# Performance work log

Hardware: AMD Instinct MI355X
Metric: run time of the kernel (lower is better)

The kernel has to match this reference:

```python
import jax, jax.numpy as jnp
import numpy as np
from jax import lax

B, BERT_DIM, Z_DIM, ODE_UNITS, T_MAX = 4096, 768, 64, 128, 512
LN_EPS = 1e-5

def _glorot(key, shape):
    fan_in, fan_out = shape[0], shape[1]
    lim = float(np.sqrt(6.0 / (fan_in + fan_out)))
    return jax.random.uniform(key, shape, jnp.float32, -lim, lim)

def setup_inputs() -> dict:
    key = jax.random.key(0)
    ks = jax.random.split(key, 16)
    inp = {
        'bert_emb': jax.random.normal(ks[0], (B, BERT_DIM), jnp.float32),
        'times': jax.random.uniform(ks[1], (B, T_MAX), jnp.float32),
        'seq_lens': jax.random.randint(ks[2], (B,), 0, T_MAX).astype(jnp.int64),
        'eps': jax.random.normal(ks[3], (B, Z_DIM), jnp.float32),
        # bert_proj: Linear(768->64) + LayerNorm(64)
        'proj_W': _glorot(ks[4], (BERT_DIM, Z_DIM)),
        'proj_b': jnp.zeros((Z_DIM,), jnp.float32),
        'ln_g': jnp.ones((Z_DIM,), jnp.float32),
        'ln_b': jnp.zeros((Z_DIM,), jnp.float32),
        # DiffusionAug
        'log_noise_std': jnp.float32(-2.0),
        'den_W1': _glorot(ks[5], (Z_DIM, 2 * Z_DIM)),
        'den_b1': jnp.zeros((2 * Z_DIM,), jnp.float32),
        'den_W2': _glorot(ks[6], (2 * Z_DIM, Z_DIM)),
        'den_b2': jnp.zeros((Z_DIM,), jnp.float32),
        # ODEFunc: Linear->Tanh->Linear->Tanh->Linear (xavier_uniform, zero bias)
        'ode_W1': _glorot(ks[7], (Z_DIM, ODE_UNITS)),
        'ode_b1': jnp.zeros((ODE_UNITS,), jnp.float32),
        'ode_W2': _glorot(ks[8], (ODE_UNITS, ODE_UNITS)),
        'ode_b2': jnp.zeros((ODE_UNITS,), jnp.float32),
        'ode_W3': _glorot(ks[9], (ODE_UNITS, Z_DIM)),
        'ode_b3': jnp.zeros((Z_DIM,), jnp.float32),
        # dec_head: Linear(64->2)
        'dec_W': _glorot(ks[10], (Z_DIM, 2)),
        'dec_b': jnp.zeros((2,), jnp.float32),
    }
    return inp

def reference(bert_emb, times, seq_lens, eps, proj_W, proj_b, ln_g, ln_b,
              log_noise_std, den_W1, den_b1, den_W2, den_b2,
              ode_W1, ode_b1, ode_W2, ode_b2, ode_W3, ode_b3, dec_W, dec_b):
    T = times.shape[1]
    # bert_proj: Linear + LayerNorm (dropout = identity in eval)
    h = bert_emb @ proj_W + proj_b
    mu = jnp.mean(h, axis=-1, keepdims=True)
    var = jnp.var(h, axis=-1, keepdims=True)
    z_clean = (h - mu) * lax.rsqrt(var + LN_EPS) * ln_g + ln_b
    # DiffusionAug: noise + denoise MLP, MSE to detached clean latent
    sigma = jax.nn.softplus(log_noise_std)
    z_noisy = z_clean + sigma * eps
    z_aug = jax.nn.silu(z_noisy @ den_W1 + den_b1) @ den_W2 + den_b2
    diff_loss = jnp.mean((z_aug - lax.stop_gradient(z_clean)) ** 2)
    # Euler ODE integration: z <- z + dt * f(z), T sequential steps
    dt = jnp.float32(1.0 / max(T, 1))
    def step(z, _):
        f = jnp.tanh(jnp.tanh(z @ ode_W1 + ode_b1) @ ode_W2 + ode_b2) @ ode_W3 + ode_b3
        z_new = z + dt * f
        return z_new, z_new
    _, zs = lax.scan(step, z_aug, None, length=T)  # zs: (T, B, z)
    traj = jnp.concatenate([z_aug[:, None, :], jnp.swapaxes(zs, 0, 1)], axis=1)  # (B, T+1, z)
    out = traj @ dec_W + dec_b  # (B, T+1, 2)
    pred_delta = out[:, :, 0]
    stop_logits = out[:, :, 1]
    return (pred_delta, stop_logits, diff_loss)
```

## Files before the change

kernel.cpp:

```cpp
#include <hip/hip_runtime.h>
#include <stdint.h>

#define NB 4096
#define NT 512
#define OT 513
#define TOTE (NB*OT)
#define LOSSOFF (2*TOTE)

typedef float  f32x4 __attribute__((ext_vector_type(4)));
typedef __fp16 f16x8 __attribute__((ext_vector_type(8)));
typedef __fp16 f16x2 __attribute__((ext_vector_type(2)));

#define MFMA(A,B,C) __builtin_amdgcn_mfma_f32_16x16x32_f16((A),(B),(C),0,0,0)

__device__ __forceinline__ void wg_barrier() {
  asm volatile("s_waitcnt lgkmcnt(0)\n\ts_barrier" ::: "memory");
}

__device__ __forceinline__ float fast_tanh(float x) {
  float e = __builtin_amdgcn_exp2f(x * 2.8853900817779268f);
  return __builtin_fmaf(-2.0f, __builtin_amdgcn_rcpf(1.0f + e), 1.0f);
}
__device__ __forceinline__ float fast_silu(float x) {
  float e = __builtin_amdgcn_exp2f(x * -1.4426950408889634f);
  return x * __builtin_amdgcn_rcpf(1.0f + e);
}
__device__ __forceinline__ uint32_t pk2(float a, float b) {
  union { f16x2 h; uint32_t u; } c;
  c.h = __builtin_amdgcn_cvt_pkrtz(a, b);
  return c.u;
}
__device__ __forceinline__ f16x8 pack8(f32x4 a, f32x4 b) {
  union { f16x8 v; f16x2 h[4]; } u;
  u.h[0] = __builtin_amdgcn_cvt_pkrtz(a.x, a.y);
  u.h[1] = __builtin_amdgcn_cvt_pkrtz(a.z, a.w);
  u.h[2] = __builtin_amdgcn_cvt_pkrtz(b.x, b.y);
  u.h[3] = __builtin_amdgcn_cvt_pkrtz(b.z, b.w);
  return u.v;
}

#define WS_WPAK (1u<<20)
#define WS_UBUF ((1u<<20) + (256u<<10))
#define WS_CBUF ((1u<<20) + (384u<<10))

__global__ void compose_kernel(const float* __restrict__ oW1, const float* __restrict__ oW3,
                               const float* __restrict__ ob3, const float* __restrict__ dW,
                               float* __restrict__ Ubuf, float* __restrict__ cbuf,
                               float* __restrict__ dout) {
  int g = blockIdx.x, tid = threadIdx.x;
  if (g < 72) {
    int e = g * 256 + tid;
    int i = e / 144, j = e - i * 144;
    float s = 0.f;
    if (j < 128) {
      #pragma unroll 4
      for (int k = 0; k < 64; k++) s = __builtin_fmaf(oW3[i * 64 + k], oW1[k * 128 + j], s);
    } else if (j < 130) {
      int cc = j - 128;
      for (int k = 0; k < 64; k++) s = __builtin_fmaf(oW3[i * 64 + k], dW[k * 2 + cc], s);
    }
    Ubuf[i * 144 + j] = s;
  } else {
    if (tid < 144) {
      float s = 0.f;
      if (tid < 128) {
        for (int k = 0; k < 64; k++) s = __builtin_fmaf(ob3[k], oW1[k * 128 + tid], s);
      } else if (tid < 130) {
        int cc = tid - 128;
        for (int k = 0; k < 64; k++) s = __builtin_fmaf(ob3[k], dW[k * 2 + cc], s);
      }
      cbuf[tid] = s;
    }
    if (tid == 255) dout[LOSSOFF] = 0.0f;
  }
}

__global__ void pack_kernel(const float* __restrict__ oW1, const float* __restrict__ oW2,
                            const float* __restrict__ dW,  const float* __restrict__ dW1,
                            const float* __restrict__ dW2, const float* __restrict__ pW,
                            const float* __restrict__ Ubuf, char* __restrict__ wdst) {
  int g = blockIdx.x * 256 + threadIdx.x;
  int fid = g >> 6, lane = g & 63;
  if (fid >= 228 || (fid >= 50 && fid < 64)) return;
  int m4 = lane & 15;
  if (fid >= 48 && fid < 50) {
    int kt = fid - 48;
    int k0 = kt * 32 + (lane >> 4) * 8;
    f16x8 out;
    #pragma unroll
    for (int j = 0; j < 8; j++) out[j] = (m4 < 2) ? (__fp16)dW[(k0 + j) * 2 + m4] : (__fp16)0.f;
    *(f16x8*)(wdst + (size_t)(fid * 64 + lane) * 16) = out;
    return;
  }
  const float* src; int Kt, M, base;
  if      (fid < 16)  { src = oW1;  Kt = 2;  M = 128; base = 0;   }
  else if (fid < 48)  { src = oW2;  Kt = 4;  M = 128; base = 16;  }
  else if (fid < 80)  { src = dW1;  Kt = 2;  M = 128; base = 64;  }
  else if (fid < 96)  { src = dW2;  Kt = 4;  M = 64;  base = 80;  }
  else if (fid < 192) { src = pW;   Kt = 24; M = 64;  base = 96;  }
  else                { src = Ubuf; Kt = 4;  M = 144; base = 192; }
  int local = fid - base;
  int mt = local / Kt, kt = local % Kt;
  int m  = mt * 16 + m4;
  int k0 = kt * 32 + (lane >> 4) * 8;
  f16x8 out;
  #pragma unroll
  for (int j = 0; j < 8; j++) out[j] = (__fp16)src[(size_t)(k0 + j) * M + m];
  *(f16x8*)(wdst + (size_t)(fid * 64 + lane) * 16) = out;
}

__global__ __launch_bounds__(512, 2) void prologue_kernel(
    const float* __restrict__ bert, const float* __restrict__ eps,
    const float* __restrict__ projb, const float* __restrict__ lng,
    const float* __restrict__ lnb,  const float* __restrict__ lns,
    const float* __restrict__ db1,  const float* __restrict__ db2,
    const char* __restrict__ wpack, float* __restrict__ wsz,
    float* __restrict__ dout) {
  __shared__ __attribute__((aligned(16))) char sZ[16 * 128];
  __shared__ __attribute__((aligned(16))) char sH[16 * 256];
  __shared__ f32x4  sScr[4 * 64];
  __shared__ float2 sMV[64];
  __shared__ float  sLsum[4];

  const int tid  = threadIdx.x;
  const int wave = tid >> 6, lane = tid & 63;
  const int q = lane >> 4, b = lane & 15;
  const int bg = blockIdx.x * 16 + b;
  const int b7 = b & 7;
  const f16x8* wp = (const f16x8*)wpack;
  const int u0 = wave * 16 + q * 4;

  const int zr0 = b * 128 + ((q    ) ^ b7) * 16;
  const int zr1 = b * 128 + ((q + 4) ^ b7) * 16;
  int hr[4];
  #pragma unroll
  for (int s = 0; s < 4; s++) hr[s] = b * 256 + ((4 * s + q) ^ b7) * 16;
  const int hw = b * 256 + (((2 * wave + (q >> 1)) ^ b7) * 16) + (q & 1) * 8;
  const int zw = b * 128 + (((2 * (wave & 3) + (q >> 1)) ^ b7) * 16) + (q & 1) * 8;

  const int mt = wave & 3, kh = wave >> 2;
  f32x4 hA = {0,0,0,0}, hB = {0,0,0,0};
  #pragma unroll 4
  for (int i = 0; i < 12; i++) {
    int kt = kh * 12 + i;
    f16x8 af = wp[(size_t)(96 + mt * 24 + kt) * 64 + lane];
    const float* bp = bert + (size_t)bg * 768 + kt * 32 + q * 8;
    f32x4 f0 = *(const f32x4*)bp;
    f32x4 f1 = *(const f32x4*)(bp + 4);
    f16x8 bf = pack8(f0, f1);
    if (i & 1) hB = MFMA(af, bf, hB); else hA = MFMA(af, bf, hA);
  }
  f32x4 hacc = hA + hB;
  if (wave >= 4) sScr[(wave - 4) * 64 + lane] = hacc;
  __syncthreads();

  f32x4 h = {0,0,0,0}, zc = {0,0,0,0};
  if (wave < 4) {
    h = hacc + sScr[wave * 64 + lane];
    h.x += projb[u0 + 0]; h.y += projb[u0 + 1];
    h.z += projb[u0 + 2]; h.w += projb[u0 + 3];
    float s1 = h.x + h.y + h.z + h.w;
    float s2 = h.x*h.x + h.y*h.y + h.z*h.z + h.w*h.w;
    s1 += __shfl_xor(s1, 16); s1 += __shfl_xor(s1, 32);
    s2 += __shfl_xor(s2, 16); s2 += __shfl_xor(s2, 32);
    if (q == 0) sMV[wave * 16 + b] = make_float2(s1, s2);
  }
  __syncthreads();
  if (wave < 4) {
    float t1 = 0.f, t2 = 0.f;
    #pragma unroll
    for (int w2 = 0; w2 < 4; w2++) { float2 m = sMV[w2 * 16 + b]; t1 += m.x; t2 += m.y; }
    float mu  = t1 * (1.0f / 64.0f);
    float var = t2 * (1.0f / 64.0f) - mu * mu;
    float rs  = rsqrtf(var + 1e-5f);
    float sigma = logf(1.0f + expf(lns[0]));
    f32x4 e = *(const f32x4*)(eps + (size_t)bg * 64 + u0);
    zc.x = __builtin_fmaf((h.x - mu) * rs, lng[u0+0], lnb[u0+0]);
    zc.y = __builtin_fmaf((h.y - mu) * rs, lng[u0+1], lnb[u0+1]);
    zc.z = __builtin_fmaf((h.z - mu) * rs, lng[u0+2], lnb[u0+2]);
    zc.w = __builtin_fmaf((h.w - mu) * rs, lng[u0+3], lnb[u0+3]);
    f32x4 zn = zc + sigma * e;
    *(uint2*)(sZ + zw) = make_uint2(pk2(zn.x, zn.y), pk2(zn.z, zn.w));
  }
  __syncthreads();
  {
    f16x8 w0 = wp[(size_t)(64 + wave * 2 + 0) * 64 + lane];
    f16x8 w1 = wp[(size_t)(64 + wave * 2 + 1) * 64 + lane];
    f16x8 bz0 = *(const f16x8*)(sZ + zr0);
    f16x8 bz1 = *(const f16x8*)(sZ + zr1);
    f32x4 bias = { db1[u0+0], db1[u0+1], db1[u0+2], db1[u0+3] };
    f32x4 acc = MFMA(w0, bz0, bias);
    acc = MFMA(w1, bz1, acc);
    *(uint2*)(sH + hw) = make_uint2(pk2(fast_silu(acc.x), fast_silu(acc.y)),
                                    pk2(fast_silu(acc.z), fast_silu(acc.w)));
  }
  __syncthreads();
  if (wave < 4) {
    f16x8 w0 = wp[(size_t)(80 + wave * 4 + 0) * 64 + lane];
    f16x8 w1 = wp[(size_t)(80 + wave * 4 + 1) * 64 + lane];
    f16x8 w2 = wp[(size_t)(80 + wave * 4 + 2) * 64 + lane];
    f16x8 w3 = wp[(size_t)(80 + wave * 4 + 3) * 64 + lane];
    f16x8 g0 = *(const f16x8*)(sH + hr[0]);
    f16x8 g1 = *(const f16x8*)(sH + hr[1]);
    f16x8 g2 = *(const f16x8*)(sH + hr[2]);
    f16x8 g3 = *(const f16x8*)(sH + hr[3]);
    f32x4 bias = { db2[u0+0], db2[u0+1], db2[u0+2], db2[u0+3] };
    const f32x4 z4 = {0,0,0,0};
    f32x4 aA = MFMA(w0, g0, bias); aA = MFMA(w1, g1, aA);
    f32x4 aB = MFMA(w2, g2, z4);   aB = MFMA(w3, g3, aB);
    f32x4 za = aA + aB;
    *(f32x4*)(wsz + (size_t)bg * 64 + u0) = za;
    f32x4 d = za - zc;
    float sl = d.x*d.x + d.y*d.y + d.z*d.z + d.w*d.w;
    const int offs[6] = {1, 2, 4, 8, 16, 32};
    #pragma unroll
    for (int i = 0; i < 6; i++) sl += __shfl_xor(sl, offs[i]);
    if (lane == 0) sLsum[wave] = sl;
  }
  __syncthreads();
  if (tid == 0)
    atomicAdd(dout + LOSSOFF,
              (sLsum[0] + sLsum[1] + sLsum[2] + sLsum[3]) * (1.0f / 262144.0f));
}

__global__ __launch_bounds__(512, 1) void ode_kernel(
    const float* __restrict__ wsz, const char* __restrict__ wpack,
    const float* __restrict__ ob1, const float* __restrict__ cbuf,
    const float* __restrict__ ob2, const float* __restrict__ decb,
    float* __restrict__ dout) {
  __shared__ __attribute__((aligned(16))) char sH1[4096];
  __shared__ __attribute__((aligned(16))) char sH2[4096];

  const int tid  = threadIdx.x;
  const int wave = tid >> 6, lane = tid & 63;
  const int q = lane >> 4, b = lane & 15;
  const f16x8* wp = (const f16x8*)wpack;
  const float dtc = 1.0f / 512.0f;
  const f32x4 zero4 = {0,0,0,0};

  int rd[4];
  #pragma unroll
  for (int kt = 0; kt < 4; kt++) rd[kt] = b * 256 + (((kt * 4 + q) ^ b) * 16);
  const int wr = b * 256 + (((wave * 2 + (q >> 1)) ^ b) * 16) + (q & 1) * 8;

  f16x8 w2f[4], uf[4], uf8[4];
  #pragma unroll
  for (int kt = 0; kt < 4; kt++) {
    w2f[kt] = wp[(size_t)(16  + wave * 4 + kt) * 64 + lane];
    uf [kt] = wp[(size_t)(192 + wave * 4 + kt) * 64 + lane];
  }
  if (wave == 7) {
    #pragma unroll
    for (int kt = 0; kt < 4; kt++)
      uf8[kt] = wp[(size_t)(192 + 32 + kt) * 64 + lane];
  }
  const f32x4 b2f = *(const f32x4*)(ob2  + wave * 16 + q * 4);
  const f32x4 cw  = *(const f32x4*)(cbuf + wave * 16 + q * 4);
  const f32x4 c8  = *(const f32x4*)(cbuf + 128 + q * 4);

  const int bg = blockIdx.x * 16 + b;
  const float* zrow = wsz + (size_t)bg * 64;
  f32x4 z0a = *(const f32x4*)(zrow + q * 8);
  f32x4 z0b = *(const f32x4*)(zrow + q * 8 + 4);
  f32x4 z1a = *(const f32x4*)(zrow + 32 + q * 8);
  f32x4 z1b = *(const f32x4*)(zrow + 32 + q * 8 + 4);
  f16x8 zf0 = pack8(z0a, z0b);
  f16x8 zf1 = pack8(z1a, z1b);

  f32x4 b1v = *(const f32x4*)(ob1 + wave * 16 + q * 4);
  f32x4 G = MFMA(wp[(size_t)(wave * 2 + 0) * 64 + lane], zf0, b1v);
  G = MFMA(wp[(size_t)(wave * 2 + 1) * 64 + lane], zf1, G);
  *(uint2*)(sH1 + wr) = make_uint2(pk2(fast_tanh(G.x), fast_tanh(G.y)),
                                   pk2(fast_tanh(G.z), fast_tanh(G.w)));

  f32x4 Gd = zero4;
  float* const outp_p = dout + (size_t)bg * OT;
  float* const outp_s = dout + (size_t)TOTE + (size_t)bg * OT;
  if (wave == 7) {
    f32x4 b1d = zero4;
    if (q == 0) { b1d.x = decb[0]; b1d.y = decb[1]; }
    Gd = MFMA(wp[(size_t)48 * 64 + lane], zf0, b1d);
    Gd = MFMA(wp[(size_t)49 * 64 + lane], zf1, Gd);
    if (q == 0) { outp_p[0] = Gd.x; outp_s[0] = Gd.y; }
  }
  wg_barrier();

  #pragma unroll 1
  for (int t = 0; t < NT; ++t) {
    f16x8 p0 = *(const f16x8*)(sH1 + rd[0]);
    f16x8 p1 = *(const f16x8*)(sH1 + rd[1]);
    f16x8 p2 = *(const f16x8*)(sH1 + rd[2]);
    f16x8 p3 = *(const f16x8*)(sH1 + rd[3]);
    f32x4 a  = MFMA(w2f[0], p0, b2f);
    a  = MFMA(w2f[1], p1, a);
    f32x4 a2 = MFMA(w2f[2], p2, zero4);
    a2 = MFMA(w2f[3], p3, a2);
    f32x4 hv = a + a2;
    *(uint2*)(sH2 + wr) = make_uint2(pk2(fast_tanh(hv.x), fast_tanh(hv.y)),
                                     pk2(fast_tanh(hv.z), fast_tanh(hv.w)));
    wg_barrier();

    f16x8 g0 = *(const f16x8*)(sH2 + rd[0]);
    f16x8 g1 = *(const f16x8*)(sH2 + rd[1]);
    f16x8 g2 = *(const f16x8*)(sH2 + rd[2]);
    f16x8 g3 = *(const f16x8*)(sH2 + rd[3]);
    f32x4 d  = MFMA(uf[0], g0, cw);
    d  = MFMA(uf[1], g1, d);
    f32x4 d2 = MFMA(uf[2], g2, zero4);
    d2 = MFMA(uf[3], g3, d2);
    G.x = __builtin_fmaf(dtc, d.x + d2.x, G.x);
    G.y = __builtin_fmaf(dtc, d.y + d2.y, G.y);
    G.z = __builtin_fmaf(dtc, d.z + d2.z, G.z);
    G.w = __builtin_fmaf(dtc, d.w + d2.w, G.w);
    *(uint2*)(sH1 + wr) = make_uint2(pk2(fast_tanh(G.x), fast_tanh(G.y)),
                                     pk2(fast_tanh(G.z), fast_tanh(G.w)));
    if (wave == 7) {
      f32x4 e  = MFMA(uf8[0], g0, c8);
      e  = MFMA(uf8[1], g1, e);
      f32x4 e2 = MFMA(uf8[2], g2, zero4);
      e2 = MFMA(uf8[3], g3, e2);
      Gd.x = __builtin_fmaf(dtc, e.x + e2.x, Gd.x);
      Gd.y = __builtin_fmaf(dtc, e.y + e2.y, Gd.y);
      if (q == 0) { outp_p[t + 1] = Gd.x; outp_s[t + 1] = Gd.y; }
    }
    wg_barrier();
  }
}

extern "C" void kernel_launch(void* const* d_in, const int* in_sizes, int n_in,
                              void* d_out, int out_size, void* d_ws, size_t ws_size,
                              hipStream_t stream) {
  const float* bert  = (const float*)d_in[0];
  const float* eps   = (const float*)d_in[3];
  const float* projW = (const float*)d_in[4];
  const float* projb = (const float*)d_in[5];
  const float* lng   = (const float*)d_in[6];
  const float* lnb   = (const float*)d_in[7];
  const float* lns   = (const float*)d_in[8];
  const float* denW1 = (const float*)d_in[9];
  const float* denb1 = (const float*)d_in[10];
  const float* denW2 = (const float*)d_in[11];
  const float* denb2 = (const float*)d_in[12];
  const float* odeW1 = (const float*)d_in[13];
  const float* odeb1 = (const float*)d_in[14];
  const float* odeW2 = (const float*)d_in[15];
  const float* odeb2 = (const float*)d_in[16];
  const float* odeW3 = (const float*)d_in[17];
  const float* odeb3 = (const float*)d_in[18];
  const float* decW  = (const float*)d_in[19];
  const float* decb  = (const float*)d_in[20];
  float* dout = (float*)d_out;

  float* wsz  = (float*)d_ws;
  char*  wpak = (char*)d_ws + WS_WPAK;
  float* Ubuf = (float*)((char*)d_ws + WS_UBUF);
  float* cbuf = (float*)((char*)d_ws + WS_CBUF);

  compose_kernel<<<73, 256, 0, stream>>>(odeW1, odeW3, odeb3, decW, Ubuf, cbuf, dout);
  pack_kernel<<<57, 256, 0, stream>>>(odeW1, odeW2, decW, denW1, denW2, projW, Ubuf, wpak);
  prologue_kernel<<<256, 512, 0, stream>>>(bert, eps, projb, lng, lnb, lns,
                                           denb1, denb2, wpak, wsz, dout);
  ode_kernel<<<256, 512, 0, stream>>>(wsz, wpak, odeb1, cbuf, odeb2, decb, dout);
}
```

Baseline: 428.5 us.

## Halve ODE block waves with two tiles per wave and fold dt into weights

The ODE kernel now runs 4 waves per block instead of 8, and each wave handles two 16-row output tiles. This cuts barrier participants and gives each wave independent MFMA chains it can interleave. The Euler step size dt is pre-multiplied into the composed U matrix and the c bias in compose_kernel. That lets the MFMA accumulate straight into the carried state G, which removes the per-step FMA scaling. The cost is more registers per wave, and the scaled fp16 weights lose some precision because small values may drop toward the subnormal range.

```diff
diff --git a/kernel.cpp b/kernel.cpp
--- a/kernel.cpp
+++ b/kernel.cpp
@@ -47,6 +47,7 @@
                                const float* __restrict__ ob3, const float* __restrict__ dW,
                                float* __restrict__ Ubuf, float* __restrict__ cbuf,
                                float* __restrict__ dout) {
+  const float dtc = 1.0f / 512.0f;
   int g = blockIdx.x, tid = threadIdx.x;
   if (g < 72) {
     int e = g * 256 + tid;
@@ -59,7 +60,7 @@
       int cc = j - 128;
       for (int k = 0; k < 64; k++) s = __builtin_fmaf(oW3[i * 64 + k], dW[k * 2 + cc], s);
     }
-    Ubuf[i * 144 + j] = s;
+    Ubuf[i * 144 + j] = s * dtc;
   } else {
     if (tid < 144) {
       float s = 0.f;
@@ -69,7 +70,7 @@
         int cc = tid - 128;
         for (int k = 0; k < 64; k++) s = __builtin_fmaf(ob3[k], dW[k * 2 + cc], s);
       }
-      cbuf[tid] = s;
+      cbuf[tid] = s * dtc;
     }
     if (tid == 255) dout[LOSSOFF] = 0.0f;
   }
@@ -223,7 +224,7 @@
               (sLsum[0] + sLsum[1] + sLsum[2] + sLsum[3]) * (1.0f / 262144.0f));
 }
 
-__global__ __launch_bounds__(512, 1) void ode_kernel(
+__global__ __launch_bounds__(256, 1) void ode_kernel(
     const float* __restrict__ wsz, const char* __restrict__ wpack,
     const float* __restrict__ ob1, const float* __restrict__ cbuf,
     const float* __restrict__ ob2, const float* __restrict__ decb,
@@ -235,28 +236,37 @@
   const int wave = tid >> 6, lane = tid & 63;
   const int q = lane >> 4, b = lane & 15;
   const f16x8* wp = (const f16x8*)wpack;
-  const float dtc = 1.0f / 512.0f;
   const f32x4 zero4 = {0,0,0,0};
 
   int rd[4];
   #pragma unroll
   for (int kt = 0; kt < 4; kt++) rd[kt] = b * 256 + (((kt * 4 + q) ^ b) * 16);
-  const int wr = b * 256 + (((wave * 2 + (q >> 1)) ^ b) * 16) + (q & 1) * 8;
-
-  f16x8 w2f[4], uf[4], uf8[4];
-  #pragma unroll
-  for (int kt = 0; kt < 4; kt++) {
-    w2f[kt] = wp[(size_t)(16  + wave * 4 + kt) * 64 + lane];
-    uf [kt] = wp[(size_t)(192 + wave * 4 + kt) * 64 + lane];
-  }
-  if (wave == 7) {
+  int wr[2];
+  #pragma unroll
+  for (int t2 = 0; t2 < 2; t2++)
+    wr[t2] = b * 256 + (((4 * wave + 2 * t2 + (q >> 1)) ^ b) * 16) + (q & 1) * 8;
+
+  f16x8 w2f[8], uf[8], uf8[4];
+  #pragma unroll
+  for (int t2 = 0; t2 < 2; t2++)
+    #pragma unroll
+    for (int kt = 0; kt < 4; kt++) {
+      w2f[t2 * 4 + kt] = wp[(size_t)(16  + (2 * wave + t2) * 4 + kt) * 64 + lane];
+      uf [t2 * 4 + kt] = wp[(size_t)(192 + (2 * wave + t2) * 4 + kt) * 64 + lane];
+    }
+  if (wave == 3) {
     #pragma unroll
     for (int kt = 0; kt < 4; kt++)
       uf8[kt] = wp[(size_t)(192 + 32 + kt) * 64 + lane];
   }
-  const f32x4 b2f = *(const f32x4*)(ob2  + wave * 16 + q * 4);
-  const f32x4 cw  = *(const f32x4*)(cbuf + wave * 16 + q * 4);
-  const f32x4 c8  = *(const f32x4*)(cbuf + 128 + q * 4);
+  f32x4 b2f[2], cw[2];
+  #pragma unroll
+  for (int t2 = 0; t2 < 2; t2++) {
+    int u0t = (2 * wave + t2) * 16 + q * 4;
+    b2f[t2] = *(const f32x4*)(ob2  + u0t);
+    cw [t2] = *(const f32x4*)(cbuf + u0t);
+  }
+  const f32x4 c8 = *(const f32x4*)(cbuf + 128 + q * 4);
 
   const int bg = blockIdx.x * 16 + b;
   const float* zrow = wsz + (size_t)bg * 64;
@@ -267,16 +277,21 @@
   f16x8 zf0 = pack8(z0a, z0b);
   f16x8 zf1 = pack8(z1a, z1b);
 
-  f32x4 b1v = *(const f32x4*)(ob1 + wave * 16 + q * 4);
-  f32x4 G = MFMA(wp[(size_t)(wave * 2 + 0) * 64 + lane], zf0, b1v);
-  G = MFMA(wp[(size_t)(wave * 2 + 1) * 64 + lane], zf1, G);
-  *(uint2*)(sH1 + wr) = make_uint2(pk2(fast_tanh(G.x), fast_tanh(G.y)),
-                                   pk2(fast_tanh(G.z), fast_tanh(G.w)));
-
+  f32x4 G[2];
+  #pragma unroll
+  for (int t2 = 0; t2 < 2; t2++) {
+    int mt = 2 * wave + t2;
+    f32x4 b1v = *(const f32x4*)(ob1 + mt * 16 + q * 4);
+    f32x4 d = MFMA(wp[(size_t)(mt * 2 + 0) * 64 + lane], zf0, b1v);
+    d = MFMA(wp[(size_t)(mt * 2 + 1) * 64 + lane], zf1, d);
+    G[t2] = d;
+    *(uint2*)(sH1 + wr[t2]) = make_uint2(pk2(fast_tanh(d.x), fast_tanh(d.y)),
+                                         pk2(fast_tanh(d.z), fast_tanh(d.w)));
+  }
   f32x4 Gd = zero4;
   float* const outp_p = dout + (size_t)bg * OT;
   float* const outp_s = dout + (size_t)TOTE + (size_t)bg * OT;
-  if (wave == 7) {
+  if (wave == 3) {
     f32x4 b1d = zero4;
     if (q == 0) { b1d.x = decb[0]; b1d.y = decb[1]; }
     Gd = MFMA(wp[(size_t)48 * 64 + lane], zf0, b1d);
@@ -291,36 +306,39 @@
     f16x8 p1 = *(const f16x8*)(sH1 + rd[1]);
     f16x8 p2 = *(const f16x8*)(sH1 + rd[2]);
     f16x8 p3 = *(const f16x8*)(sH1 + rd[3]);
-    f32x4 a  = MFMA(w2f[0], p0, b2f);
-    a  = MFMA(w2f[1], p1, a);
-    f32x4 a2 = MFMA(w2f[2], p2, zero4);
-    a2 = MFMA(w2f[3], p3, a2);
-    f32x4 hv = a + a2;
-    *(uint2*)(sH2 + wr) = make_uint2(pk2(fast_tanh(hv.x), fast_tanh(hv.y)),
-                                     pk2(fast_tanh(hv.z), fast_tanh(hv.w)));
+    #pragma unroll
+    for (int t2 = 0; t2 < 2; t2++) {
+      f32x4 a  = MFMA(w2f[t2*4+0], p0, b2f[t2]);
+      a  = MFMA(w2f[t2*4+1], p1, a);
+      f32x4 a2 = MFMA(w2f[t2*4+2], p2, zero4);
+      a2 = MFMA(w2f[t2*4+3], p3, a2);
+      f32x4 hv = a + a2;
+      *(uint2*)(sH2 + wr[t2]) = make_uint2(pk2(fast_tanh(hv.x), fast_tanh(hv.y)),
+                                           pk2(fast_tanh(hv.z), fast_tanh(hv.w)));
+    }
     wg_barrier();
 
     f16x8 g0 = *(const f16x8*)(sH2 + rd[0]);
     f16x8 g1 = *(const f16x8*)(sH2 + rd[1]);
     f16x8 g2 = *(const f16x8*)(sH2 + rd[2]);
     f16x8 g3 = *(const f16x8*)(sH2 + rd[3]);
-    f32x4 d  = MFMA(uf[0], g0, cw);
-    d  = MFMA(uf[1], g1, d);
-    f32x4 d2 = MFMA(uf[2], g2, zero4);
-    d2 = MFMA(uf[3], g3, d2);
-    G.x = __builtin_fmaf(dtc, d.x + d2.x, G.x);
-    G.y = __builtin_fmaf(dtc, d.y + d2.y, G.y);
-    G.z = __builtin_fmaf(dtc, d.z + d2.z, G.z);
-    G.w = __builtin_fmaf(dtc, d.w + d2.w, G.w);
-    *(uint2*)(sH1 + wr) = make_uint2(pk2(fast_tanh(G.x), fast_tanh(G.y)),
-                                     pk2(fast_tanh(G.z), fast_tanh(G.w)));
-    if (wave == 7) {
-      f32x4 e  = MFMA(uf8[0], g0, c8);
+    #pragma unroll
+    for (int t2 = 0; t2 < 2; t2++) {
+      f32x4 d  = MFMA(uf[t2*4+0], g0, G[t2]);
+      d  = MFMA(uf[t2*4+1], g1, d);
+      f32x4 d2 = MFMA(uf[t2*4+2], g2, zero4);
+      d2 = MFMA(uf[t2*4+3], g3, d2);
+      f32x4 Gn = d + d2 + cw[t2];
+      G[t2] = Gn;
+      *(uint2*)(sH1 + wr[t2]) = make_uint2(pk2(fast_tanh(Gn.x), fast_tanh(Gn.y)),
+                                           pk2(fast_tanh(Gn.z), fast_tanh(Gn.w)));
+    }
+    if (wave == 3) {
+      f32x4 e  = MFMA(uf8[0], g0, Gd);
       e  = MFMA(uf8[1], g1, e);
       f32x4 e2 = MFMA(uf8[2], g2, zero4);
       e2 = MFMA(uf8[3], g3, e2);
-      Gd.x = __builtin_fmaf(dtc, e.x + e2.x, Gd.x);
-      Gd.y = __builtin_fmaf(dtc, e.y + e2.y, Gd.y);
+      Gd = e + e2 + c8;
       if (q == 0) { outp_p[t + 1] = Gd.x; outp_s[t + 1] = Gd.y; }
     }
     wg_barrier();
@@ -360,5 +378,5 @@
   pack_kernel<<<57, 256, 0, stream>>>(odeW1, odeW2, decW, denW1, denW2, projW, Ubuf, wpak);
   prologue_kernel<<<256, 512, 0, stream>>>(bert, eps, projb, lng, lnb, lns,
                                            denb1, denb2, wpak, wsz, dout);
-  ode_kernel<<<256, 512, 0, stream>>>(wsz, wpak, odeb1, cbuf, odeb2, decb, dout);
-}
+  ode_kernel<<<256, 256, 0, stream>>>(wsz, wpak, odeb1, cbuf, odeb2, decb, dout);
+}
```

New measurement: 499.0 us. 16.4% more time.

## Fuse prep and main kernels, fold dt into composed weights, keep z in LDS

Applied to the files above, without the earlier changes.

Merges the compose and pack kernels into one prep kernel that computes the dt-scaled composed W3·W1 weights directly into packed fp16 form. The prologue and ODE kernels are fused, so the augmented latent is passed through shared memory instead of a global round-trip. The Euler update is folded into the MFMA accumulator by pre-scaling the weights and bias with dt, which removes per-step FMAs. The goal is fewer launches and less memory traffic. The cost is more fp16 rounding on the small scaled weights and on the stored latent.

```diff
diff --git a/kernel.cpp b/kernel.cpp
--- a/kernel.cpp
+++ b/kernel.cpp
@@ -39,28 +39,17 @@
   return u.v;
 }
 
-#define WS_WPAK (1u<<20)
-#define WS_UBUF ((1u<<20) + (256u<<10))
-#define WS_CBUF ((1u<<20) + (384u<<10))
-
-__global__ void compose_kernel(const float* __restrict__ oW1, const float* __restrict__ oW3,
-                               const float* __restrict__ ob3, const float* __restrict__ dW,
-                               float* __restrict__ Ubuf, float* __restrict__ cbuf,
-                               float* __restrict__ dout) {
-  int g = blockIdx.x, tid = threadIdx.x;
-  if (g < 72) {
-    int e = g * 256 + tid;
-    int i = e / 144, j = e - i * 144;
-    float s = 0.f;
-    if (j < 128) {
-      #pragma unroll 4
-      for (int k = 0; k < 64; k++) s = __builtin_fmaf(oW3[i * 64 + k], oW1[k * 128 + j], s);
-    } else if (j < 130) {
-      int cc = j - 128;
-      for (int k = 0; k < 64; k++) s = __builtin_fmaf(oW3[i * 64 + k], dW[k * 2 + cc], s);
-    }
-    Ubuf[i * 144 + j] = s;
-  } else {
+#define WS_CBUF (256u<<10)
+
+__global__ void prep_kernel(const float* __restrict__ oW1, const float* __restrict__ oW2,
+                            const float* __restrict__ dW,  const float* __restrict__ dW1,
+                            const float* __restrict__ dW2, const float* __restrict__ pW,
+                            const float* __restrict__ oW3, const float* __restrict__ ob3,
+                            char* __restrict__ wdst, float* __restrict__ cbuf,
+                            float* __restrict__ dout) {
+  const float dtc = 1.0f / 512.0f;
+  if (blockIdx.x == 57) {
+    int tid = threadIdx.x;
     if (tid < 144) {
       float s = 0.f;
       if (tid < 128) {
@@ -69,58 +58,77 @@
         int cc = tid - 128;
         for (int k = 0; k < 64; k++) s = __builtin_fmaf(ob3[k], dW[k * 2 + cc], s);
       }
-      cbuf[tid] = s;
+      cbuf[tid] = s * dtc;
     }
     if (tid == 255) dout[LOSSOFF] = 0.0f;
-  }
-}
-
-__global__ void pack_kernel(const float* __restrict__ oW1, const float* __restrict__ oW2,
-                            const float* __restrict__ dW,  const float* __restrict__ dW1,
-                            const float* __restrict__ dW2, const float* __restrict__ pW,
-                            const float* __restrict__ Ubuf, char* __restrict__ wdst) {
+    return;
+  }
   int g = blockIdx.x * 256 + threadIdx.x;
   int fid = g >> 6, lane = g & 63;
-  if (fid >= 228 || (fid >= 50 && fid < 64)) return;
+  if (fid >= 50 && fid < 64) return;
   int m4 = lane & 15;
+  int k0 = (lane >> 4) * 8;
   if (fid >= 48 && fid < 50) {
     int kt = fid - 48;
-    int k0 = kt * 32 + (lane >> 4) * 8;
+    int kb = kt * 32 + k0;
     f16x8 out;
     #pragma unroll
-    for (int j = 0; j < 8; j++) out[j] = (m4 < 2) ? (__fp16)dW[(k0 + j) * 2 + m4] : (__fp16)0.f;
+    for (int j = 0; j < 8; j++) out[j] = (m4 < 2) ? (__fp16)dW[(kb + j) * 2 + m4] : (__fp16)0.f;
     *(f16x8*)(wdst + (size_t)(fid * 64 + lane) * 16) = out;
     return;
   }
+  if (fid >= 192) {
+    int local = fid - 192;
+    int mt = local >> 2, kt = local & 3;
+    int m  = mt * 16 + m4;
+    int kb = kt * 32 + k0;
+    f16x8 out;
+    #pragma unroll
+    for (int j = 0; j < 8; j++) {
+      int k = kb + j;
+      float s = 0.f;
+      if (m < 128) {
+        #pragma unroll 4
+        for (int i = 0; i < 64; i++) s = __builtin_fmaf(oW3[k * 64 + i], oW1[i * 128 + m], s);
+      } else if (m < 130) {
+        for (int i = 0; i < 64; i++) s = __builtin_fmaf(oW3[k * 64 + i], dW[i * 2 + (m - 128)], s);
+      }
+      out[j] = (__fp16)(s * dtc);
+    }
+    *(f16x8*)(wdst + (size_t)(fid * 64 + lane) * 16) = out;
+    return;
+  }
   const float* src; int Kt, M, base;
-  if      (fid < 16)  { src = oW1;  Kt = 2;  M = 128; base = 0;   }
-  else if (fid < 48)  { src = oW2;  Kt = 4;  M = 128; base = 16;  }
-  else if (fid < 80)  { src = dW1;  Kt = 2;  M = 128; base = 64;  }
-  else if (fid < 96)  { src = dW2;  Kt = 4;  M = 64;  base = 80;  }
-  else if (fid < 192) { src = pW;   Kt = 24; M = 64;  base = 96;  }
-  else                { src = Ubuf; Kt = 4;  M = 144; base = 192; }
+  if      (fid < 16)  { src = oW1;  Kt = 2;  M = 128; base = 0;  }
+  else if (fid < 48)  { src = oW2;  Kt = 4;  M = 128; base = 16; }
+  else if (fid < 80)  { src = dW1;  Kt = 2;  M = 128; base = 64; }
+  else if (fid < 96)  { src = dW2;  Kt = 4;  M = 64;  base = 80; }
+  else                { src = pW;   Kt = 24; M = 64;  base = 96; }
   int local = fid - base;
   int mt = local / Kt, kt = local % Kt;
   int m  = mt * 16 + m4;
-  int k0 = kt * 32 + (lane >> 4) * 8;
+  int kb = kt * 32 + k0;
   f16x8 out;
   #pragma unroll
-  for (int j = 0; j < 8; j++) out[j] = (__fp16)src[(size_t)(k0 + j) * M + m];
+  for (int j = 0; j < 8; j++) out[j] = (__fp16)src[(size_t)(kb + j) * M + m];
   *(f16x8*)(wdst + (size_t)(fid * 64 + lane) * 16) = out;
 }
 
-__global__ __launch_bounds__(512, 2) void prologue_kernel(
+__global__ __launch_bounds__(512, 1) void main_kernel(
     const float* __restrict__ bert, const float* __restrict__ eps,
     const float* __restrict__ projb, const float* __restrict__ lng,
     const float* __restrict__ lnb,  const float* __restrict__ lns,
     const float* __restrict__ db1,  const float* __restrict__ db2,
-    const char* __restrict__ wpack, float* __restrict__ wsz,
-    float* __restrict__ dout) {
+    const float* __restrict__ ob1,  const float* __restrict__ ob2,
+    const float* __restrict__ decb, const char* __restrict__ wpack,
+    const float* __restrict__ cbuf, float* __restrict__ dout) {
   __shared__ __attribute__((aligned(16))) char sZ[16 * 128];
   __shared__ __attribute__((aligned(16))) char sH[16 * 256];
   __shared__ f32x4  sScr[4 * 64];
   __shared__ float2 sMV[64];
   __shared__ float  sLsum[4];
+  __shared__ __attribute__((aligned(16))) char sH1[4096];
+  __shared__ __attribute__((aligned(16))) char sH2[4096];
 
   const int tid  = threadIdx.x;
   const int wave = tid >> 6, lane = tid & 63;
@@ -129,6 +137,7 @@
   const int b7 = b & 7;
   const f16x8* wp = (const f16x8*)wpack;
   const int u0 = wave * 16 + q * 4;
+  const f32x4 zero4 = {0,0,0,0};
 
   const int zr0 = b * 128 + ((q    ) ^ b7) * 16;
   const int zr1 = b * 128 + ((q + 4) ^ b7) * 16;
@@ -138,105 +147,90 @@
   const int hw = b * 256 + (((2 * wave + (q >> 1)) ^ b7) * 16) + (q & 1) * 8;
   const int zw = b * 128 + (((2 * (wave & 3) + (q >> 1)) ^ b7) * 16) + (q & 1) * 8;
 
-  const int mt = wave & 3, kh = wave >> 2;
-  f32x4 hA = {0,0,0,0}, hB = {0,0,0,0};
-  #pragma unroll 4
-  for (int i = 0; i < 12; i++) {
-    int kt = kh * 12 + i;
-    f16x8 af = wp[(size_t)(96 + mt * 24 + kt) * 64 + lane];
-    const float* bp = bert + (size_t)bg * 768 + kt * 32 + q * 8;
-    f32x4 f0 = *(const f32x4*)bp;
-    f32x4 f1 = *(const f32x4*)(bp + 4);
-    f16x8 bf = pack8(f0, f1);
-    if (i & 1) hB = MFMA(af, bf, hB); else hA = MFMA(af, bf, hA);
-  }
-  f32x4 hacc = hA + hB;
-  if (wave >= 4) sScr[(wave - 4) * 64 + lane] = hacc;
-  __syncthreads();
-
-  f32x4 h = {0,0,0,0}, zc = {0,0,0,0};
-  if (wave < 4) {
-    h = hacc + sScr[wave * 64 + lane];
-    h.x += projb[u0 + 0]; h.y += projb[u0 + 1];
-    h.z += projb[u0 + 2]; h.w += projb[u0 + 3];
-    float s1 = h.x + h.y + h.z + h.w;
-    float s2 = h.x*h.x + h.y*h.y + h.z*h.z + h.w*h.w;
-    s1 += __shfl_xor(s1, 16); s1 += __shfl_xor(s1, 32);
-    s2 += __shfl_xor(s2, 16); s2 += __shfl_xor(s2, 32);
-    if (q == 0) sMV[wave * 16 + b] = make_float2(s1, s2);
-  }
-  __syncthreads();
-  if (wave < 4) {
-    float t1 = 0.f, t2 = 0.f;
-    #pragma unroll
-    for (int w2 = 0; w2 < 4; w2++) { float2 m = sMV[w2 * 16 + b]; t1 += m.x; t2 += m.y; }
-    float mu  = t1 * (1.0f / 64.0f);
-    float var = t2 * (1.0f / 64.0f) - mu * mu;
-    float rs  = rsqrtf(var + 1e-5f);
-    float sigma = logf(1.0f + expf(lns[0]));
-    f32x4 e = *(const f32x4*)(eps + (size_t)bg * 64 + u0);
-    zc.x = __builtin_fmaf((h.x - mu) * rs, lng[u0+0], lnb[u0+0]);
-    zc.y = __builtin_fmaf((h.y - mu) * rs, lng[u0+1], lnb[u0+1]);
-    zc.z = __builtin_fmaf((h.z - mu) * rs, lng[u0+2], lnb[u0+2]);
-    zc.w = __builtin_fmaf((h.w - mu) * rs, lng[u0+3], lnb[u0+3]);
-    f32x4 zn = zc + sigma * e;
-    *(uint2*)(sZ + zw) = make_uint2(pk2(zn.x, zn.y), pk2(zn.z, zn.w));
-  }
-  __syncthreads();
   {
-    f16x8 w0 = wp[(size_t)(64 + wave * 2 + 0) * 64 + lane];
-    f16x8 w1 = wp[(size_t)(64 + wave * 2 + 1) * 64 + lane];
-    f16x8 bz0 = *(const f16x8*)(sZ + zr0);
-    f16x8 bz1 = *(const f16x8*)(sZ + zr1);
-    f32x4 bias = { db1[u0+0], db1[u0+1], db1[u0+2], db1[u0+3] };
-    f32x4 acc = MFMA(w0, bz0, bias);
-    acc = MFMA(w1, bz1, acc);
-    *(uint2*)(sH + hw) = make_uint2(pk2(fast_silu(acc.x), fast_silu(acc.y)),
-                                    pk2(fast_silu(acc.z), fast_silu(acc.w)));
-  }
-  __syncthreads();
-  if (wave < 4) {
-    f16x8 w0 = wp[(size_t)(80 + wave * 4 + 0) * 64 + lane];
-    f16x8 w1 = wp[(size_t)(80 + wave * 4 + 1) * 64 + lane];
-    f16x8 w2 = wp[(size_t)(80 + wave * 4 + 2) * 64 + lane];
-    f16x8 w3 = wp[(size_t)(80 + wave * 4 + 3) * 64 + lane];
-    f16x8 g0 = *(const f16x8*)(sH + hr[0]);
-    f16x8 g1 = *(const f16x8*)(sH + hr[1]);
-    f16x8 g2 = *(const f16x8*)(sH + hr[2]);
-    f16x8 g3 = *(const f16x8*)(sH + hr[3]);
-    f32x4 bias = { db2[u0+0], db2[u0+1], db2[u0+2], db2[u0+3] };
-    const f32x4 z4 = {0,0,0,0};
-    f32x4 aA = MFMA(w0, g0, bias); aA = MFMA(w1, g1, aA);
-    f32x4 aB = MFMA(w2, g2, z4);   aB = MFMA(w3, g3, aB);
-    f32x4 za = aA + aB;
-    *(f32x4*)(wsz + (size_t)bg * 64 + u0) = za;
-    f32x4 d = za - zc;
-    float sl = d.x*d.x + d.y*d.y + d.z*d.z + d.w*d.w;
-    const int offs[6] = {1, 2, 4, 8, 16, 32};
-    #pragma unroll
-    for (int i = 0; i < 6; i++) sl += __shfl_xor(sl, offs[i]);
-    if (lane == 0) sLsum[wave] = sl;
-  }
-  __syncthreads();
-  if (tid == 0)
-    atomicAdd(dout + LOSSOFF,
-              (sLsum[0] + sLsum[1] + sLsum[2] + sLsum[3]) * (1.0f / 262144.0f));
-}
-
-__global__ __launch_bounds__(512, 1) void ode_kernel(
-    const float* __restrict__ wsz, const char* __restrict__ wpack,
-    const float* __restrict__ ob1, const float* __restrict__ cbuf,
-    const float* __restrict__ ob2, const float* __restrict__ decb,
-    float* __restrict__ dout) {
-  __shared__ __attribute__((aligned(16))) char sH1[4096];
-  __shared__ __attribute__((aligned(16))) char sH2[4096];
-
-  const int tid  = threadIdx.x;
-  const int wave = tid >> 6, lane = tid & 63;
-  const int q = lane >> 4, b = lane & 15;
-  const f16x8* wp = (const f16x8*)wpack;
-  const float dtc = 1.0f / 512.0f;
-  const f32x4 zero4 = {0,0,0,0};
+    const int mt = wave & 3, kh = wave >> 2;
+    f32x4 hA = {0,0,0,0}, hB = {0,0,0,0};
+    #pragma unroll 4
+    for (int i = 0; i < 12; i++) {
+      int kt = kh * 12 + i;
+      f16x8 af = wp[(size_t)(96 + mt * 24 + kt) * 64 + lane];
+      const float* bp = bert + (size_t)bg * 768 + kt * 32 + q * 8;
+      f32x4 f0 = *(const f32x4*)bp;
+      f32x4 f1 = *(const f32x4*)(bp + 4);
+      f16x8 bf = pack8(f0, f1);
+      if (i & 1) hB = MFMA(af, bf, hB); else hA = MFMA(af, bf, hA);
+    }
+    f32x4 hacc = hA + hB;
+    if (wave >= 4) sScr[(wave - 4) * 64 + lane] = hacc;
+    __syncthreads();
+
+    f32x4 h = {0,0,0,0}, zc = {0,0,0,0};
+    if (wave < 4) {
+      h = hacc + sScr[wave * 64 + lane];
+      h.x += projb[u0 + 0]; h.y += projb[u0 + 1];
+      h.z += projb[u0 + 2]; h.w += projb[u0 + 3];
+      float s1 = h.x + h.y + h.z + h.w;
+      float s2 = h.x*h.x + h.y*h.y + h.z*h.z + h.w*h.w;
+      s1 += __shfl_xor(s1, 16); s1 += __shfl_xor(s1, 32);
+      s2 += __shfl_xor(s2, 16); s2 += __shfl_xor(s2, 32);
+      if (q == 0) sMV[wave * 16 + b] = make_float2(s1, s2);
+    }
+    __syncthreads();
+    if (wave < 4) {
+      float t1 = 0.f, t2 = 0.f;
+      #pragma unroll
+      for (int w2 = 0; w2 < 4; w2++) { float2 m = sMV[w2 * 16 + b]; t1 += m.x; t2 += m.y; }
+      float mu  = t1 * (1.0f / 64.0f);
+      float var = t2 * (1.0f / 64.0f) - mu * mu;
+      float rs  = rsqrtf(var + 1e-5f);
+      float sigma = logf(1.0f + expf(lns[0]));
+      f32x4 e = *(const f32x4*)(eps + (size_t)bg * 64 + u0);
+      zc.x = __builtin_fmaf((h.x - mu) * rs, lng[u0+0], lnb[u0+0]);
+      zc.y = __builtin_fmaf((h.y - mu) * rs, lng[u0+1], lnb[u0+1]);
+      zc.z = __builtin_fmaf((h.z - mu) * rs, lng[u0+2], lnb[u0+2]);
+      zc.w = __builtin_fmaf((h.w - mu) * rs, lng[u0+3], lnb[u0+3]);
+      f32x4 zn = zc + sigma * e;
+      *(uint2*)(sZ + zw) = make_uint2(pk2(zn.x, zn.y), pk2(zn.z, zn.w));
+    }
+    __syncthreads();
+    {
+      f16x8 w0 = wp[(size_t)(64 + wave * 2 + 0) * 64 + lane];
+      f16x8 w1 = wp[(size_t)(64 + wave * 2 + 1) * 64 + lane];
+      f16x8 bz0 = *(const f16x8*)(sZ + zr0);
+      f16x8 bz1 = *(const f16x8*)(sZ + zr1);
+      f32x4 bias = { db1[u0+0], db1[u0+1], db1[u0+2], db1[u0+3] };
+      f32x4 acc = MFMA(w0, bz0, bias);
+      acc = MFMA(w1, bz1, acc);
+      *(uint2*)(sH + hw) = make_uint2(pk2(fast_silu(acc.x), fast_silu(acc.y)),
+                                      pk2(fast_silu(acc.z), fast_silu(acc.w)));
+    }
+    __syncthreads();
+    if (wave < 4) {
+      f16x8 w0 = wp[(size_t)(80 + wave * 4 + 0) * 64 + lane];
+      f16x8 w1 = wp[(size_t)(80 + wave * 4 + 1) * 64 + lane];
+      f16x8 w2 = wp[(size_t)(80 + wave * 4 + 2) * 64 + lane];
+      f16x8 w3 = wp[(size_t)(80 + wave * 4 + 3) * 64 + lane];
+      f16x8 g0 = *(const f16x8*)(sH + hr[0]);
+      f16x8 g1 = *(const f16x8*)(sH + hr[1]);
+      f16x8 g2 = *(const f16x8*)(sH + hr[2]);
+      f16x8 g3 = *(const f16x8*)(sH + hr[3]);
+      f32x4 bias = { db2[u0+0], db2[u0+1], db2[u0+2], db2[u0+3] };
+      f32x4 aA = MFMA(w0, g0, bias); aA = MFMA(w1, g1, aA);
+      f32x4 aB = MFMA(w2, g2, zero4); aB = MFMA(w3, g3, aB);
+      f32x4 za = aA + aB;
+      *(uint2*)(sZ + zw) = make_uint2(pk2(za.x, za.y), pk2(za.z, za.w));
+      f32x4 d = za - zc;
+      float sl = d.x*d.x + d.y*d.y + d.z*d.z + d.w*d.w;
+      const int offs[6] = {1, 2, 4, 8, 16, 32};
+      #pragma unroll
+      for (int i = 0; i < 6; i++) sl += __shfl_xor(sl, offs[i]);
+      if (lane == 0) sLsum[wave] = sl;
+    }
+    __syncthreads();
+    if (tid == 0)
+      atomicAdd(dout + LOSSOFF,
+                (sLsum[0] + sLsum[1] + sLsum[2] + sLsum[3]) * (1.0f / 262144.0f));
+  }
 
   int rd[4];
   #pragma unroll
@@ -258,15 +252,8 @@
   const f32x4 cw  = *(const f32x4*)(cbuf + wave * 16 + q * 4);
   const f32x4 c8  = *(const f32x4*)(cbuf + 128 + q * 4);
 
-  const int bg = blockIdx.x * 16 + b;
-  const float* zrow = wsz + (size_t)bg * 64;
-  f32x4 z0a = *(const f32x4*)(zrow + q * 8);
-  f32x4 z0b = *(const f32x4*)(zrow + q * 8 + 4);
-  f32x4 z1a = *(const f32x4*)(zrow + 32 + q * 8);
-  f32x4 z1b = *(const f32x4*)(zrow + 32 + q * 8 + 4);
-  f16x8 zf0 = pack8(z0a, z0b);
-  f16x8 zf1 = pack8(z1a, z1b);
-
+  f16x8 zf0 = *(const f16x8*)(sZ + zr0);
+  f16x8 zf1 = *(const f16x8*)(sZ + zr1);
   f32x4 b1v = *(const f32x4*)(ob1 + wave * 16 + q * 4);
   f32x4 G = MFMA(wp[(size_t)(wave * 2 + 0) * 64 + lane], zf0, b1v);
   G = MFMA(wp[(size_t)(wave * 2 + 1) * 64 + lane], zf1, G);
@@ -304,23 +291,19 @@
     f16x8 g1 = *(const f16x8*)(sH2 + rd[1]);
     f16x8 g2 = *(const f16x8*)(sH2 + rd[2]);
     f16x8 g3 = *(const f16x8*)(sH2 + rd[3]);
-    f32x4 d  = MFMA(uf[0], g0, cw);
+    f32x4 d  = MFMA(uf[0], g0, G);
     d  = MFMA(uf[1], g1, d);
-    f32x4 d2 = MFMA(uf[2], g2, zero4);
+    f32x4 d2 = MFMA(uf[2], g2, cw);
     d2 = MFMA(uf[3], g3, d2);
-    G.x = __builtin_fmaf(dtc, d.x + d2.x, G.x);
-    G.y = __builtin_fmaf(dtc, d.y + d2.y, G.y);
-    G.z = __builtin_fmaf(dtc, d.z + d2.z, G.z);
-    G.w = __builtin_fmaf(dtc, d.w + d2.w, G.w);
+    G = d + d2;
     *(uint2*)(sH1 + wr) = make_uint2(pk2(fast_tanh(G.x), fast_tanh(G.y)),
                                      pk2(fast_tanh(G.z), fast_tanh(G.w)));
     if (wave == 7) {
-      f32x4 e  = MFMA(uf8[0], g0, c8);
+      f32x4 e  = MFMA(uf8[0], g0, Gd);
       e  = MFMA(uf8[1], g1, e);
-      f32x4 e2 = MFMA(uf8[2], g2, zero4);
+      f32x4 e2 = MFMA(uf8[2], g2, c8);
       e2 = MFMA(uf8[3], g3, e2);
-      Gd.x = __builtin_fmaf(dtc, e.x + e2.x, Gd.x);
-      Gd.y = __builtin_fmaf(dtc, e.y + e2.y, Gd.y);
+      Gd = e + e2;
       if (q == 0) { outp_p[t + 1] = Gd.x; outp_s[t + 1] = Gd.y; }
     }
     wg_barrier();
@@ -351,14 +334,12 @@
   const float* decb  = (const float*)d_in[20];
   float* dout = (float*)d_out;
 
-  float* wsz  = (float*)d_ws;
-  char*  wpak = (char*)d_ws + WS_WPAK;
-  float* Ubuf = (float*)((char*)d_ws + WS_UBUF);
+  char*  wpak = (char*)d_ws;
   float* cbuf = (float*)((char*)d_ws + WS_CBUF);
 
-  compose_kernel<<<73, 256, 0, stream>>>(odeW1, odeW3, odeb3, decW, Ubuf, cbuf, dout);
-  pack_kernel<<<57, 256, 0, stream>>>(odeW1, odeW2, decW, denW1, denW2, projW, Ubuf, wpak);
-  prologue_kernel<<<256, 512, 0, stream>>>(bert, eps, projb, lng, lnb, lns,
-                                           denb1, denb2, wpak, wsz, dout);
-  ode_kernel<<<256, 512, 0, stream>>>(wsz, wpak, odeb1, cbuf, odeb2, decb, dout);
-}
+  prep_kernel<<<58, 256, 0, stream>>>(odeW1, odeW2, decW, denW1, denW2, projW,
+                                      odeW3, odeb3, wpak, cbuf, dout);
+  main_kernel<<<256, 512, 0, stream>>>(bert, eps, projb, lng, lnb, lns,
+                                       denb1, denb2, odeb1, odeb2, decb,
+                                       wpak, cbuf, dout);
+}
```

Measured after the change: 435.0 us (median of 2 runs). No clear change (+1.5%).
